# Optimization experiments

Measured on AMD Instinct MI355X. Metric: run time of the kernel, lower is better.

Reference implementation:

```python
import jax, jax.numpy as jnp
import numpy as np
from jax import lax

DIM = 192
HEADS = 4
K = 3
PAD = 1


def conv2d(x, w, groups=1, pad=0):
    # x: [B,C,H,W], w: [O, C//groups, kh, kw]
    return lax.conv_general_dilated(
        x, w, window_strides=(1, 1), padding=[(pad, pad), (pad, pad)],
        dimension_numbers=("NCHW", "OIHW", "NCHW"), feature_group_count=groups)


def setup_inputs() -> dict:
    key = jax.random.key(0)
    ks = jax.random.split(key, 8)
    b, c, h, w = 2, DIM, 256, 256
    x = jax.random.normal(ks[0], (b, c, h, w), dtype=jnp.float32)
    y = jax.random.normal(ks[1], (b, c, h, w), dtype=jnp.float32)
    s = 0.05
    qk_w = jax.random.normal(ks[2], (2 * DIM, DIM, 1, 1), dtype=jnp.float32) * s
    qk_dw_w = jax.random.normal(ks[3], (2 * DIM, 1, K, K), dtype=jnp.float32) * s  # depthwise, groups=2*dim
    v_w = jax.random.normal(ks[4], (DIM, DIM, 1, 1), dtype=jnp.float32) * s
    v_dw_w = jax.random.normal(ks[5], (DIM, DIM, K, K), dtype=jnp.float32) * s    # NOTE: not grouped in source
    proj_w = jax.random.normal(ks[6], (DIM, DIM, 1, 1), dtype=jnp.float32) * s
    temperature = jnp.ones((HEADS, 1, 1), dtype=jnp.float32)
    return {"x": x, "y": y, "qk_w": qk_w, "qk_dw_w": qk_dw_w, "v_w": v_w,
            "v_dw_w": v_dw_w, "proj_w": proj_w, "temperature": temperature}


def reference(x, y, qk_w, qk_dw_w, v_w, v_dw_w, proj_w, temperature):
    b, c, h, w = x.shape
    hd = c // HEADS  # channels per head
    qk = conv2d(conv2d(x, qk_w), qk_dw_w, groups=2 * DIM, pad=PAD)  # [b, 2c, h, w]
    q, k = jnp.split(qk, 2, axis=1)
    v = conv2d(conv2d(y, v_w), v_dw_w, pad=PAD)  # full conv (groups=1), per source

    def to_heads(t):
        return t.reshape(b, HEADS, hd, h * w)  # b head c (hw)

    q, k, v = to_heads(q), to_heads(k), to_heads(v)
    # L2 normalize along spatial (last) axis, eps matches torch F.normalize (1e-12)
    q = q / jnp.maximum(jnp.linalg.norm(q, axis=-1, keepdims=True), 1e-12)
    k = k / jnp.maximum(jnp.linalg.norm(k, axis=-1, keepdims=True), 1e-12)
    attn = jnp.einsum("bhcn,bhdn->bhcd", q, k) * temperature  # [b, head, c, c]
    attn = jax.nn.softmax(attn, axis=-1)
    out = jnp.einsum("bhcd,bhdn->bhcn", attn, v)
    out = out.reshape(b, c, h, w)
    return conv2d(out, proj_w)
```

## Files before the change

### kernel.cpp

```cpp
#include <hip/hip_runtime.h>
#include <hip/hip_bf16.h>

#define NPIX 65536
#define CDIM 192
#define C2   384
#define HEADS 4
#define HD   48
#define PROW 258
#define XTROWS (PROW * PROW)

typedef float f32x4 __attribute__((ext_vector_type(4)));
typedef short short8 __attribute__((ext_vector_type(8)));

__device__ __forceinline__ unsigned short f2bf(float x) {
  union { float f; unsigned u; } v; v.f = x;
  unsigned r = v.u + 0x7fff + ((v.u >> 16) & 1);
  return (unsigned short)(r >> 16);
}
__device__ __forceinline__ float bf2f(unsigned short x) {
  union { unsigned u; float f; } v; v.u = ((unsigned)x) << 16;
  return v.f;
}
__device__ __forceinline__ int f4(int r) { return (r ^ (r >> 2)) & 3; }

__device__ __forceinline__ void gload_lds16(const void* g, void* l) {
  __builtin_amdgcn_global_load_lds(
      (const __attribute__((address_space(1))) unsigned int*)g,
      (__attribute__((address_space(3))) unsigned int*)l, 16, 0, 0);
}

__global__ __launch_bounds__(256) void castw_kernel(
    const float* __restrict__ qkw, const float* __restrict__ vw,
    unsigned short* __restrict__ wqk, unsigned short* __restrict__ wv) {
  int i = blockIdx.x * 256 + threadIdx.x;
  if (i < C2 * CDIM) wqk[i] = f2bf(qkw[i]);
  if (i < CDIM * CDIM) wv[i] = f2bf(vw[i]);
}

__global__ __launch_bounds__(512) void qk_mfma_kernel(
    const float* __restrict__ X, const unsigned short* __restrict__ W,
    unsigned short* __restrict__ Out) {
  const int px0 = blockIdx.x * 128;
  __shared__ __align__(16) char smem[67584];
  short* sA = (short*)smem;
  short* sB = (short*)(smem + 49152);
  const int t = threadIdx.x;
  const int lane = t & 63;
  const int wid = t >> 6;
  const int cpp = t & 31;
  const int pg = t >> 5;
  const int l15 = lane & 15;
  const int l4 = lane >> 4;

  f32x4 acc[3][8];
#pragma unroll
  for (int mi = 0; mi < 3; ++mi)
#pragma unroll
    for (int ni = 0; ni < 8; ++ni) acc[mi][ni] = (f32x4){0.f, 0.f, 0.f, 0.f};

  for (int k0 = 0; k0 < CDIM; k0 += 64) {
#pragma unroll
    for (int i = 0; i < 6; ++i) {
      int g = i * 512 + t;
      int row = g >> 3, ck = g & 7;
      gload_lds16(W + (size_t)row * CDIM + k0 + ((ck ^ (row & 7)) * 8),
                  (char*)sA + ((size_t)i * 512 + (t & ~63)) * 16);
    }
    {
      const float* xp = X + (size_t)(k0 + 2 * cpp) * NPIX + px0 + 8 * pg;
      float4 a0 = *(const float4*)xp;
      float4 a1 = *(const float4*)(xp + 4);
      float4 b0 = *(const float4*)(xp + NPIX);
      float4 b1 = *(const float4*)(xp + NPIX + 4);
      float av[8] = {a0.x, a0.y, a0.z, a0.w, a1.x, a1.y, a1.z, a1.w};
      float bv[8] = {b0.x, b0.y, b0.z, b0.w, b1.x, b1.y, b1.z, b1.w};
#pragma unroll
      for (int i = 0; i < 8; ++i) {
        unsigned d = (unsigned)f2bf(av[i]) | ((unsigned)f2bf(bv[i]) << 16);
        *(unsigned*)&sB[(8 * pg + i) * 72 + 2 * cpp] = d;
      }
    }
    asm volatile("s_waitcnt vmcnt(0)");
    __syncthreads();
#pragma unroll
    for (int kk = 0; kk < 2; ++kk) {
      short8 af[3], bf[8];
#pragma unroll
      for (int mi = 0; mi < 3; ++mi) {
        int row = wid * 48 + mi * 16 + l15;
        af[mi] = *(const short8*)&sA[row * 64 +
                                     (((kk * 4 + l4) ^ (row & 7)) * 8)];
      }
#pragma unroll
      for (int ni = 0; ni < 8; ++ni)
        bf[ni] = *(const short8*)&sB[(ni * 16 + l15) * 72 + (kk * 4 + l4) * 8];
#pragma unroll
      for (int mi = 0; mi < 3; ++mi)
#pragma unroll
        for (int ni = 0; ni < 8; ++ni)
          acc[mi][ni] = __builtin_amdgcn_mfma_f32_16x16x32_bf16(
              af[mi], bf[ni], acc[mi][ni], 0, 0, 0);
    }
    __syncthreads();
  }
  short* zones = (short*)smem;
  short* zone = zones + wid * 2176;
#pragma unroll
  for (int mi = 0; mi < 3; ++mi) {
#pragma unroll
    for (int ni = 0; ni < 8; ++ni)
#pragma unroll
      for (int rg = 0; rg < 4; ++rg)
        zone[(l4 * 4 + rg) * 136 + ni * 16 + l15] =
            (short)f2bf(acc[mi][ni][rg]);
    asm volatile("s_waitcnt lgkmcnt(0)" ::: "memory");
    __builtin_amdgcn_sched_barrier(0);
#pragma unroll
    for (int it = 0; it < 4; ++it) {
      int e = it * 64 + lane;
      int ol = e >> 4, pxg = e & 15;
      short8 vv = *(const short8*)&zone[ol * 136 + pxg * 8];
      *(short8*)&Out[(size_t)(wid * 48 + mi * 16 + ol) * NPIX + px0 + pxg * 8] = vv;
    }
    asm volatile("s_waitcnt lgkmcnt(0)" ::: "memory");
    __builtin_amdgcn_sched_barrier(0);
  }
}

__global__ __launch_bounds__(256, 4) void v_mfma_kernel(
    const float* __restrict__ Y0, const unsigned short* __restrict__ W,
    unsigned short* __restrict__ Xt0) {
  const int b = blockIdx.y;
  const float* Y = Y0 + (size_t)b * CDIM * NPIX;
  unsigned short* Xt = Xt0 + (size_t)b * XTROWS * CDIM;
  const int px0 = blockIdx.x * 64;
  const int h = px0 >> 8;
  const int w0 = px0 & 255;
  __shared__ short sX[64 * 40];
  __shared__ short sW[CDIM * 32];
  __shared__ short sZ[4 * 16 * 104];
  const int t = threadIdx.x;
  const int lane = t & 63;
  const int wid = t >> 6;
  const int cp = t & 15;
  const int pg = t >> 4;
  const int l15 = lane & 15;
  const int l4 = lane >> 4;

  f32x4 acc[12];
#pragma unroll
  for (int ni = 0; ni < 12; ++ni) acc[ni] = (f32x4){0.f, 0.f, 0.f, 0.f};

  for (int k0 = 0; k0 < CDIM; k0 += 32) {
#pragma unroll
    for (int i = 0; i < 3; ++i) {
      int e = i * 256 + t;
      int oc = e >> 2, kg = e & 3;
      gload_lds16(W + (size_t)oc * CDIM + k0 + (kg ^ f4(oc)) * 8,
                  (char*)sW + ((size_t)i * 256 + (t & ~63)) * 16);
    }
    {
      const float* xp = Y + (size_t)(k0 + 2 * cp) * NPIX + px0 + 4 * pg;
      float4 a = *(const float4*)xp;
      float4 b2 = *(const float4*)(xp + NPIX);
      float av[4] = {a.x, a.y, a.z, a.w};
      float bv[4] = {b2.x, b2.y, b2.z, b2.w};
#pragma unroll
      for (int i = 0; i < 4; ++i) {
        unsigned d = (unsigned)f2bf(av[i]) | ((unsigned)f2bf(bv[i]) << 16);
        *(unsigned*)&sX[(4 * pg + i) * 40 + 2 * cp] = d;
      }
    }
    asm volatile("s_waitcnt vmcnt(0)");
    __syncthreads();
    short8 af = *(const short8*)&sX[(wid * 16 + l15) * 40 + l4 * 8];
    short8 bf[12];
#pragma unroll
    for (int ni = 0; ni < 12; ++ni) {
      int row = ni * 16 + l15;
      bf[ni] = *(const short8*)&sW[row * 32 + (l4 ^ f4(row)) * 8];
    }
#pragma unroll
    for (int ni = 0; ni < 12; ++ni)
      acc[ni] = __builtin_amdgcn_mfma_f32_16x16x32_bf16(af, bf[ni], acc[ni],
                                                        0, 0, 0);
    __syncthreads();
  }
  short* zone = sZ + wid * (16 * 104);
#pragma unroll
  for (int oh = 0; oh < 2; ++oh) {
#pragma unroll
    for (int ni = 0; ni < 6; ++ni)
#pragma unroll
      for (int rg = 0; rg < 4; ++rg)
        zone[(l4 * 4 + rg) * 104 + ni * 16 + l15] =
            (short)f2bf(acc[oh * 6 + ni][rg]);
    asm volatile("s_waitcnt lgkmcnt(0)" ::: "memory");
    __builtin_amdgcn_sched_barrier(0);
#pragma unroll
    for (int it = 0; it < 3; ++it) {
      int e = it * 64 + lane;
      int pl = e / 12, cg = e % 12;
      short8 vv = *(const short8*)&zone[pl * 104 + cg * 8];
      size_t xrow = (size_t)(h + 1) * PROW + (w0 + wid * 16 + pl + 1);
      *(short8*)&Xt[xrow * CDIM + oh * 96 + cg * 8] = vv;
    }
    asm volatile("s_waitcnt lgkmcnt(0)" ::: "memory");
    __builtin_amdgcn_sched_barrier(0);
  }
}

__global__ __launch_bounds__(128) void border_zero_kernel(
    unsigned short* __restrict__ Xt0) {
  unsigned short* Xt = Xt0 + (size_t)blockIdx.y * XTROWS * CDIM;
  int pos = blockIdx.x;
  size_t row;
  if (pos < 258) row = pos;
  else if (pos < 516) row = (size_t)257 * PROW + (pos - 258);
  else { int i = pos - 516; row = (size_t)(1 + (i >> 1)) * PROW + ((i & 1) ? 257 : 0); }
  unsigned* p = (unsigned*)(Xt + row * CDIM);
  if (threadIdx.x < 96) p[threadIdx.x] = 0;
}

__global__ __launch_bounds__(256) void dwgram_kernel(
    const unsigned short* __restrict__ qkb, const float* __restrict__ dw,
    float* __restrict__ gpart_b, float* __restrict__ ssp_b) {
  const int head = blockIdx.y;
  const int braw = blockIdx.x;
  const int blk = (braw & 7) * 16 + (braw >> 3);
  const int t = threadIdx.x;
  const int lane = t & 63;
  const int wid = t >> 6;

  __shared__ __align__(16) char smem[38400];
  short* zone = (short*)smem + wid * (96 * 40);

  const int qrow0 = HD * head, krow0 = CDIM + HD * head;
  const int p0 = (lane & 1) * 16;
  const int c0 = (lane >> 1) * 3;

  float wr[3][9];
#pragma unroll
  for (int j = 0; j < 3; ++j) {
    int ch = c0 + j;
    int srow = (ch < HD) ? (qrow0 + ch) : (krow0 + ch - HD);
#pragma unroll
    for (int i = 0; i < 9; ++i) wr[j][i] = dw[srow * 9 + i];
  }

  f32x4 acc[3][3];
#pragma unroll
  for (int mi = 0; mi < 3; ++mi)
#pragma unroll
    for (int nj = 0; nj < 3; ++nj) acc[mi][nj] = (f32x4){0.f, 0.f, 0.f, 0.f};
  float ss[3] = {0.f, 0.f, 0.f};

  const int pxbase = blk * 512 + wid * 128;
  for (int s = 0; s < 4; ++s) {
    const int px0 = pxbase + s * 32;
    const int hr = px0 >> 8;
    const int col0 = px0 & 255;
    const int cl = col0 + p0;
#pragma unroll
    for (int j = 0; j < 3; ++j) {
      int ch = c0 + j;
      int srow = (ch < HD) ? (qrow0 + ch) : (krow0 + ch - HD);
      const unsigned short* ip = qkb + (size_t)srow * NPIX;
      float win[3][18];
#pragma unroll
      for (int r = 0; r < 3; ++r) {
        int ir = hr - 1 + r;
        if ((unsigned)ir < 256u) {
          const unsigned short* rp = ip + ir * 256 + cl;
          short8 v0 = *(const short8*)rp;
          short8 v1 = *(const short8*)(rp + 8);
#pragma unroll
          for (int q = 0; q < 8; ++q) {
            win[r][1 + q] = bf2f((unsigned short)v0[q]);
            win[r][9 + q] = bf2f((unsigned short)v1[q]);
          }
          win[r][0]  = (cl > 0)        ? bf2f(rp[-1]) : 0.f;
          win[r][17] = (cl + 16 < 256) ? bf2f(rp[16]) : 0.f;
        } else {
#pragma unroll
          for (int q = 0; q < 18; ++q) win[r][q] = 0.f;
        }
      }
      unsigned pk[8];
#pragma unroll
      for (int p = 0; p < 16; ++p) {
        float sacc = 0.f;
#pragma unroll
        for (int r = 0; r < 3; ++r)
#pragma unroll
          for (int c = 0; c < 3; ++c) sacc += wr[j][r * 3 + c] * win[r][p + c];
        ss[j] += sacc * sacc;
        unsigned short bb = f2bf(sacc);
        if (p & 1) pk[p >> 1] |= ((unsigned)bb << 16);
        else       pk[p >> 1] = bb;
      }
      unsigned* zp = (unsigned*)&zone[ch * 40 + p0];
#pragma unroll
      for (int q = 0; q < 8; ++q) zp[q] = pk[q];
    }
    asm volatile("s_waitcnt lgkmcnt(0)" ::: "memory");
    __builtin_amdgcn_sched_barrier(0);
    short8 qf[3], kf[3];
#pragma unroll
    for (int mi = 0; mi < 3; ++mi)
      qf[mi] = *(const short8*)&zone[(mi * 16 + (lane & 15)) * 40 +
                                     (lane >> 4) * 8];
#pragma unroll
    for (int nj = 0; nj < 3; ++nj)
      kf[nj] = *(const short8*)&zone[(HD + nj * 16 + (lane & 15)) * 40 +
                                     (lane >> 4) * 8];
#pragma unroll
    for (int mi = 0; mi < 3; ++mi)
#pragma unroll
      for (int nj = 0; nj < 3; ++nj)
        acc[mi][nj] = __builtin_amdgcn_mfma_f32_16x16x32_bf16(
            qf[mi], kf[nj], acc[mi][nj], 0, 0, 0);
    asm volatile("s_waitcnt lgkmcnt(0)" ::: "memory");
    __builtin_amdgcn_sched_barrier(0);
  }
  __syncthreads();
  float* red   = (float*)smem;
  float* ssred = (float*)(smem + 36864);
#pragma unroll
  for (int mi = 0; mi < 3; ++mi)
#pragma unroll
    for (int nj = 0; nj < 3; ++nj) {
      int kj = nj * 16 + (lane & 15);
#pragma unroll
      for (int rg = 0; rg < 4; ++rg) {
        int qi = mi * 16 + (lane >> 4) * 4 + rg;
        red[wid * 2304 + qi * HD + kj] = acc[mi][nj][rg];
      }
    }
#pragma unroll
  for (int j = 0; j < 3; ++j) {
    float sj = ss[j] + __shfl_xor(ss[j], 1);
    if ((lane & 1) == 0) ssred[wid * 96 + c0 + j] = sj;
  }
  __syncthreads();
  float* gp = gpart_b + (size_t)(head * 128 + blk) * (HD * HD);
  for (int e = t; e < HD * HD; e += 256)
    gp[e] = red[e] + red[2304 + e] + red[4608 + e] + red[6912 + e];
  if (t < 96)
    ssp_b[(size_t)(head * 128 + blk) * 96 + t] =
        ssred[t] + ssred[96 + t] + ssred[192 + t] + ssred[288 + t];
}

__global__ __launch_bounds__(128) void normred_kernel(
    const float* __restrict__ ssp, float* __restrict__ norms) {
  int idx = blockIdx.x;
  int bh = idx / 96, ch = idx % 96;
  int l = threadIdx.x;
  float s = ssp[((size_t)bh * 128 + l) * 96 + ch];
#pragma unroll
  for (int off = 32; off; off >>= 1) s += __shfl_down(s, off);
  __shared__ float red[2];
  if ((l & 63) == 0) red[l >> 6] = s;
  __syncthreads();
  if (l == 0) {
    int b = bh >> 2, hh = bh & 3;
    int g = b * C2 + (ch < HD ? hh * HD + ch : CDIM + hh * HD + ch - HD);
    norms[g] = sqrtf(red[0] + red[1]);
  }
}

__global__ __launch_bounds__(256) void gramred_kernel(
    const float* __restrict__ part, float* __restrict__ logits) {
  int ij = blockIdx.x * 256 + threadIdx.x;
  int bh = blockIdx.y;
  if (ij >= HD * HD) return;
  const float* pp = part + (size_t)bh * 128 * (HD * HD);
  float s = 0.f;
  for (int sp = 0; sp < 128; ++sp) s += pp[(size_t)sp * (HD * HD) + ij];
  logits[(size_t)bh * (HD * HD) + ij] = s;
}

__global__ __launch_bounds__(64) void softmax_kernel(
    float* __restrict__ logits, const float* __restrict__ norms,
    const float* __restrict__ temperature) {
  int hh = blockIdx.x, b = blockIdx.y;
  int i = threadIdx.x;
  if (i >= HD) return;
  const float eps = 1e-12f;
  float temp = temperature[hh];
  float nq = fmaxf(norms[b * C2 + HD * hh + i], eps);
  float* row = logits + (((size_t)b * HEADS + hh) * HD + i) * HD;
  float vals[48];
  float mx = -1e30f;
#pragma unroll
  for (int j = 0; j < HD; ++j) {
    float nk = fmaxf(norms[b * C2 + CDIM + HD * hh + j], eps);
    float v = row[j] / (nq * nk) * temp;
    vals[j] = v;
    mx = fmaxf(mx, v);
  }
  float sum = 0.f;
#pragma unroll
  for (int j = 0; j < HD; ++j) {
    vals[j] = expf(vals[j] - mx);
    sum += vals[j];
  }
  float inv = 1.f / sum;
#pragma unroll
  for (int j = 0; j < HD; ++j) row[j] = vals[j] * inv;
}

__global__ __launch_bounds__(256) void buildM_kernel(
    const float* __restrict__ attn, const float* __restrict__ projw,
    float* __restrict__ M) {
  int idx = blockIdx.x * 256 + threadIdx.x;
  if (idx >= 2 * CDIM * CDIM) return;
  int d = idx % CDIM;
  int oc = (idx / CDIM) % CDIM;
  int b = idx / (CDIM * CDIM);
  int hh = d / HD, dd = d % HD;
  const float* arow = attn + ((size_t)b * HEADS + hh) * HD * HD;
  float s = 0.f;
#pragma unroll
  for (int c = 0; c < HD; ++c)
    s += projw[oc * CDIM + HD * hh + c] * arow[c * HD + dd];
  M[idx] = s;
}

__global__ __launch_bounds__(256) void wtrans_kernel(
    const float* __restrict__ M, const float* __restrict__ Wv,
    unsigned short* __restrict__ Wb) {
  const int ocb = blockIdx.x * 4;
  const int ec0 = blockIdx.y * 432;
  const int b = blockIdx.z;
  __shared__ float sM[4][CDIM];
  for (int i = threadIdx.x; i < 4 * CDIM; i += 256)
    sM[i / CDIM][i % CDIM] =
        M[((size_t)b * CDIM + ocb + i / CDIM) * CDIM + (i % CDIM)];
  __syncthreads();
  for (int e = ec0 + threadIdx.x; e < ec0 + 432; e += 256) {
    float a0 = 0.f, a1 = 0.f, a2 = 0.f, a3 = 0.f;
#pragma unroll 4
    for (int d = 0; d < CDIM; ++d) {
      float wv = Wv[(size_t)d * (CDIM * 9) + e];
      a0 += sM[0][d] * wv; a1 += sM[1][d] * wv;
      a2 += sM[2][d] * wv; a3 += sM[3][d] * wv;
    }
    int ic = e / 9, tap = e % 9;
    size_t base = (((size_t)b * 9 + tap) * CDIM) * CDIM + ic;
    Wb[base + (size_t)(ocb + 0) * CDIM] = f2bf(a0);
    Wb[base + (size_t)(ocb + 1) * CDIM] = f2bf(a1);
    Wb[base + (size_t)(ocb + 2) * CDIM] = f2bf(a2);
    Wb[base + (size_t)(ocb + 3) * CDIM] = f2bf(a3);
  }
}

__global__ __launch_bounds__(256, 3) void conv3x3_mfma_kernel(
    const unsigned short* __restrict__ Xt,
    const unsigned short* __restrict__ Wb,
    float* __restrict__ out) {
  const int d = blockIdx.x;
  const int xcd = d & 7;
  const int j = d >> 3;
  const int h = xcd * 32 + j / 3;
  const int oc0 = (j % 3) * 64;

  __shared__ __align__(16) short sA[3 * 64 * 32];
  __shared__ __align__(16) short sB[2][258 * 32];

  const int t = threadIdx.x;
  const int lane = t & 63;
  const int wid = t >> 6;
  const int l15 = lane & 15;
  const int l4 = lane >> 4;

  f32x4 acc[4][4];
#pragma unroll
  for (int mi = 0; mi < 4; ++mi)
#pragma unroll
    for (int ni = 0; ni < 4; ++ni) acc[mi][ni] = (f32x4){0.f, 0.f, 0.f, 0.f};

#define STAGE_A(sidx)                                                        \
  {                                                                          \
    const int ra_ = (sidx) / 6;                                              \
    const int ica_ = ((sidx) % 6) * 32;                                      \
    _Pragma("unroll")                                                        \
    for (int i = 0; i < 3; ++i) {                                            \
      int g = i * 256 + t;                                                   \
      int row = g >> 2, ck = g & 3;                                          \
      int tap = row >> 6, oc = row & 63;                                     \
      gload_lds16(Wb + ((size_t)(ra_ * 3 + tap) * CDIM + oc0 + oc) * CDIM +  \
                      ica_ + (ck ^ f4(row)) * 8,                             \
                  (char*)sA + (size_t)(i * 256 + wid * 64) * 16);            \
    }                                                                        \
  }
#define STAGE_B(sidx, bi)                                                    \
  {                                                                          \
    const int rs_ = (sidx) / 6;                                              \
    const int ics_ = ((sidx) % 6) * 32;                                      \
    const unsigned short* bsrc =                                             \
        Xt + (size_t)(h + rs_) * PROW * CDIM + ics_;                         \
    _Pragma("unroll")                                                        \
    for (int i = 0; i < 4; ++i) {                                            \
      int g = i * 256 + t;                                                   \
      int row = g >> 2, ck = g & 3;                                          \
      gload_lds16(bsrc + (size_t)row * CDIM + (ck ^ f4(row)) * 8,            \
                  (char*)sB[bi] + (size_t)(i * 256 + wid * 64) * 16);        \
    }                                                                        \
    { int g = 1024 + wid * 2 + lane;                                         \
      int row = g >> 2, ck = g & 3;                                          \
      if (lane < 2)                                                          \
        gload_lds16(bsrc + (size_t)row * CDIM + (ck ^ f4(row)) * 8,          \
                    (char*)sB[bi] + (size_t)(1024 + wid * 2) * 16);          \
    }                                                                        \
  }

  STAGE_A(0);
  STAGE_B(0, 0);
  asm volatile("s_waitcnt vmcnt(0)" ::: "memory");
  __syncthreads();

  int cur = 0;
  for (int s = 0; s < 18; ++s) {
    short8 af_[3][4];
#pragma unroll
    for (int c = 0; c < 3; ++c)
#pragma unroll
      for (int mi = 0; mi < 4; ++mi) {
        int row = c * 64 + mi * 16 + l15;
        af_[c][mi] = *(const short8*)&sA[row * 32 + (l4 ^ f4(row)) * 8];
      }
    __syncthreads();
    if (s < 17) {
      STAGE_A(s + 1);
      STAGE_B(s + 1, cur ^ 1);
    }
#pragma unroll
    for (int c = 0; c < 3; ++c) {
      short8 bf[4];
#pragma unroll
      for (int ni = 0; ni < 4; ++ni) {
        int row = wid * 64 + ni * 16 + l15 + c;
        bf[ni] = *(const short8*)&sB[cur][row * 32 + (l4 ^ f4(row)) * 8];
      }
#pragma unroll
      for (int mi = 0; mi < 4; ++mi)
#pragma unroll
        for (int ni = 0; ni < 4; ++ni)
          acc[mi][ni] = __builtin_amdgcn_mfma_f32_16x16x32_bf16(
              af_[c][mi], bf[ni], acc[mi][ni], 0, 0, 0);
    }
    asm volatile("s_waitcnt vmcnt(0)" ::: "memory");
    __syncthreads();
    cur ^= 1;
  }
#undef STAGE_A
#undef STAGE_B
#pragma unroll
  for (int mi = 0; mi < 4; ++mi) {
    int ocl = oc0 + mi * 16 + l4 * 4;
#pragma unroll
    for (int ni = 0; ni < 4; ++ni) {
      int wloc = wid * 64 + ni * 16 + l15;
#pragma unroll
      for (int rg = 0; rg < 4; ++rg)
        out[(size_t)(ocl + rg) * NPIX + h * 256 + wloc] = acc[mi][ni][rg];
    }
  }
}

extern "C" void kernel_launch(void* const* d_in, const int* in_sizes, int n_in,
                              void* d_out, int out_size, void* d_ws, size_t ws_size,
                              hipStream_t stream) {
  const float* x          = (const float*)d_in[0];
  const float* y          = (const float*)d_in[1];
  const float* qk_w       = (const float*)d_in[2];
  const float* qk_dw_w    = (const float*)d_in[3];
  const float* v_w        = (const float*)d_in[4];
  const float* v_dw_w     = (const float*)d_in[5];
  const float* proj_w     = (const float*)d_in[6];
  const float* temperature= (const float*)d_in[7];
  float* out = (float*)d_out;

  unsigned short* XtA = (unsigned short*)d_ws;
  unsigned short* qkb = XtA;
  float* gpart  = (float*)(XtA + (size_t)2 * XTROWS * CDIM);
  float* ssp    = gpart + (size_t)8 * 128 * HD * HD;
  float* norms  = ssp + (size_t)8 * 128 * 96;
  float* logits = norms + 768;
  float* M      = logits + 2 * HEADS * HD * HD;
  unsigned short* wqk = (unsigned short*)(M + 2 * CDIM * CDIM);
  unsigned short* wv  = wqk + C2 * CDIM;
  unsigned short* Wb  = wv + CDIM * CDIM;
  size_t needB = (size_t)((char*)(Wb + (size_t)2 * 9 * CDIM * CDIM) - (char*)d_ws);
  if (ws_size < needB) return;

  castw_kernel<<<dim3(288), dim3(256), 0, stream>>>(qk_w, v_w, wqk, wv);

  for (int b = 0; b < 2; ++b) {
    qk_mfma_kernel<<<dim3(512), dim3(512), 0, stream>>>(
        x + (size_t)b * CDIM * NPIX, wqk, qkb);
    dwgram_kernel<<<dim3(128, HEADS), dim3(256), 0, stream>>>(
        qkb, qk_dw_w,
        gpart + (size_t)b * HEADS * 128 * HD * HD,
        ssp + (size_t)b * HEADS * 128 * 96);
  }
  normred_kernel<<<dim3(768), dim3(128), 0, stream>>>(ssp, norms);
  gramred_kernel<<<dim3(9, 8), dim3(256), 0, stream>>>(gpart, logits);
  softmax_kernel<<<dim3(4, 2), dim3(64), 0, stream>>>(logits, norms, temperature);
  buildM_kernel<<<dim3(288), dim3(256), 0, stream>>>(logits, proj_w, M);
  wtrans_kernel<<<dim3(48, 4, 2), dim3(256), 0, stream>>>(M, v_dw_w, Wb);

  border_zero_kernel<<<dim3(1028, 2), dim3(128), 0, stream>>>(XtA);
  v_mfma_kernel<<<dim3(1024, 2), dim3(256), 0, stream>>>(y, wv, XtA);
  for (int b = 0; b < 2; ++b) {
    conv3x3_mfma_kernel<<<dim3(768), dim3(256), 0, stream>>>(
        XtA + (size_t)b * XTROWS * CDIM,
        Wb + (size_t)b * 9 * CDIM * CDIM,
        out + (size_t)b * CDIM * NPIX);
  }
}
```

Measured before the change: 373.5 us.

## Double-buffer LDS in v 1x1 conv MFMA kernel to overlap loads

Splits the v-projection kernel's shared memory into two ping-pong buffers for the X and W tiles. Global loads for the next K-slice are issued before the MFMAs on the current slice, and the bf16 conversion is written afterwards. This removes one barrier per iteration and hides global latency behind compute. In exchange LDS use grows to about 34 KB per block, which may lower occupancy below the four blocks per CU the launch bounds target. The epilogue staging zone is aliased onto the W buffer region.

```diff
diff --git a/kernel.cpp b/kernel.cpp
--- a/kernel.cpp
+++ b/kernel.cpp
@@ -136,9 +136,7 @@
   const int px0 = blockIdx.x * 64;
   const int h = px0 >> 8;
   const int w0 = px0 & 255;
-  __shared__ short sX[64 * 40];
-  __shared__ short sW[CDIM * 32];
-  __shared__ short sZ[4 * 16 * 104];
+  __shared__ __align__(16) char smem[34816];
   const int t = threadIdx.x;
   const int lane = t & 63;
   const int wid = t >> 6;
@@ -151,42 +149,77 @@
 #pragma unroll
   for (int ni = 0; ni < 12; ++ni) acc[ni] = (f32x4){0.f, 0.f, 0.f, 0.f};
 
-  for (int k0 = 0; k0 < CDIM; k0 += 32) {
-#pragma unroll
-    for (int i = 0; i < 3; ++i) {
-      int e = i * 256 + t;
-      int oc = e >> 2, kg = e & 3;
-      gload_lds16(W + (size_t)oc * CDIM + k0 + (kg ^ f4(oc)) * 8,
-                  (char*)sW + ((size_t)i * 256 + (t & ~63)) * 16);
+#define SXB(p) ((short*)(smem + (p) * 5120))
+#define SWB(p) ((short*)(smem + 10240 + (p) * 12288))
+
+#define STAGE_W(k0_, p_)                                                     \
+  {                                                                          \
+    _Pragma("unroll")                                                        \
+    for (int i = 0; i < 3; ++i) {                                            \
+      int e = i * 256 + t;                                                   \
+      int oc = e >> 2, kg = e & 3;                                           \
+      gload_lds16(W + (size_t)oc * CDIM + (k0_) + (kg ^ f4(oc)) * 8,         \
+                  (char*)SWB(p_) + ((size_t)i * 256 + (t & ~63)) * 16);      \
+    }                                                                        \
+  }
+
+  float4 ya, yb;
+#define LOAD_Y(k0_)                                                          \
+  {                                                                          \
+    const float* xp = Y + (size_t)((k0_) + 2 * cp) * NPIX + px0 + 4 * pg;    \
+    ya = *(const float4*)xp;                                                 \
+    yb = *(const float4*)(xp + NPIX);                                        \
+  }
+#define WRITE_X(p_)                                                          \
+  {                                                                          \
+    float av[4] = {ya.x, ya.y, ya.z, ya.w};                                  \
+    float bv[4] = {yb.x, yb.y, yb.z, yb.w};                                  \
+    short* sx = SXB(p_);                                                     \
+    _Pragma("unroll")                                                        \
+    for (int i = 0; i < 4; ++i) {                                            \
+      unsigned d = (unsigned)f2bf(av[i]) | ((unsigned)f2bf(bv[i]) << 16);    \
+      *(unsigned*)&sx[(4 * pg + i) * 40 + 2 * cp] = d;                       \
+    }                                                                        \
+  }
+
+  LOAD_Y(0);
+  STAGE_W(0, 0);
+  WRITE_X(0);
+  asm volatile("s_waitcnt vmcnt(0)" ::: "memory");
+  __syncthreads();
+
+  for (int k = 0; k < 6; ++k) {
+    const int p = k & 1;
+    if (k < 5) {
+      LOAD_Y((k + 1) * 32);
+      STAGE_W((k + 1) * 32, p ^ 1);
     }
     {
-      const float* xp = Y + (size_t)(k0 + 2 * cp) * NPIX + px0 + 4 * pg;
-      float4 a = *(const float4*)xp;
-      float4 b2 = *(const float4*)(xp + NPIX);
-      float av[4] = {a.x, a.y, a.z, a.w};
-      float bv[4] = {b2.x, b2.y, b2.z, b2.w};
-#pragma unroll
-      for (int i = 0; i < 4; ++i) {
-        unsigned d = (unsigned)f2bf(av[i]) | ((unsigned)f2bf(bv[i]) << 16);
-        *(unsigned*)&sX[(4 * pg + i) * 40 + 2 * cp] = d;
-      }
-    }
-    asm volatile("s_waitcnt vmcnt(0)");
+      short* sx = SXB(p);
+      short* sw = SWB(p);
+      short8 af = *(const short8*)&sx[(wid * 16 + l15) * 40 + l4 * 8];
+      short8 bf[12];
+#pragma unroll
+      for (int ni = 0; ni < 12; ++ni) {
+        int row = ni * 16 + l15;
+        bf[ni] = *(const short8*)&sw[row * 32 + (l4 ^ f4(row)) * 8];
+      }
+#pragma unroll
+      for (int ni = 0; ni < 12; ++ni)
+        acc[ni] = __builtin_amdgcn_mfma_f32_16x16x32_bf16(af, bf[ni], acc[ni],
+                                                          0, 0, 0);
+    }
+    if (k < 5) WRITE_X(p ^ 1);
+    asm volatile("s_waitcnt vmcnt(0)" ::: "memory");
     __syncthreads();
-    short8 af = *(const short8*)&sX[(wid * 16 + l15) * 40 + l4 * 8];
-    short8 bf[12];
-#pragma unroll
-    for (int ni = 0; ni < 12; ++ni) {
-      int row = ni * 16 + l15;
-      bf[ni] = *(const short8*)&sW[row * 32 + (l4 ^ f4(row)) * 8];
-    }
-#pragma unroll
-    for (int ni = 0; ni < 12; ++ni)
-      acc[ni] = __builtin_amdgcn_mfma_f32_16x16x32_bf16(af, bf[ni], acc[ni],
-                                                        0, 0, 0);
-    __syncthreads();
-  }
-  short* zone = sZ + wid * (16 * 104);
+  }
+#undef STAGE_W
+#undef LOAD_Y
+#undef WRITE_X
+#undef SXB
+#undef SWB
+
+  short* zone = (short*)(smem + 10240) + wid * (16 * 104);
 #pragma unroll
   for (int oh = 0; oh < 2; ++oh) {
 #pragma unroll
```

Measured after the change: 369.9 us. No clear change (-1.0%).
